# Performance work log

Measured on AMD Instinct MI355X. Metric: run time of the kernel, lower is better.

The kernel has to match this reference:

```python
import jax, jax.numpy as jnp
import numpy as np

# Bone edge list (0-indexed) from _calc_length_single, in original order.
_BONES = np.array([
    (3, 2), (2, 20), (20, 8), (8, 9), (9, 10), (10, 11),
    (20, 4), (4, 5), (5, 6), (6, 7),
    (20, 1), (1, 0), (0, 16), (16, 17), (17, 18), (18, 19),
    (0, 12), (12, 13), (13, 14), (14, 15),
], dtype=np.int32)
_A = jnp.asarray(_BONES[:, 0])
_B = jnp.asarray(_BONES[:, 1])


def _bone_lengths(joints):
    # joints: [B, 21, 3] -> [B, 20]
    diff = joints[:, _A, :] - joints[:, _B, :]
    return jnp.linalg.norm(diff, axis=-1)


def setup_inputs() -> dict:
    key = jax.random.key(0)
    k1, k2 = jax.random.split(key)
    B = 524288
    pred_joints = jax.random.normal(k1, (B, 21, 3), dtype=jnp.float32)
    gt_joints = jax.random.normal(k2, (B, 21, 3), dtype=jnp.float32)
    return {"pred_joints": pred_joints, "gt_joints": gt_joints}


def reference(pred_joints, gt_joints):
    pred_len = _bone_lengths(pred_joints)   # [B, 20]
    gt_len = _bone_lengths(gt_joints)       # [B, 20]
    rel = jnp.abs(pred_len - gt_len) / gt_len
    # mean over 20 bones per sample, then mean over batch == global mean
    return jnp.mean(rel)
```

## Files before the change

### kernel.cpp

```cpp
#include <hip/hip_runtime.h>
#include <hip/hip_bf16.h>


#define TILE_BYTES   16128
#define TILE_PAD_F   4096
#define NBLOCKS      512

static constexpr int JT0[7] = {3,2,2,20,8,9,10};
static constexpr int JT1[7] = {10,11,20,4,5,6,7};
static constexpr int JT2[7] = {20,1,1,0,16,17,18};
static constexpr int JT3[7] = {18,19,0,12,13,14,15};
static constexpr int EA[5] = {0,2,3,4,5};
static constexpr int EB[5] = {1,3,4,5,6};

typedef __attribute__((address_space(1))) const void gvoid_t;
typedef __attribute__((address_space(3))) void lvoid_t;

template<int G>
__device__ __forceinline__ float bone_group(const float* __restrict__ SP,
                                            const float* __restrict__ SG) {
    float px[7], py[7], pz[7], qx[7], qy[7], qz[7];
    #pragma unroll
    for (int k = 0; k < 7; ++k) {
        const int o = 3 * ((G == 0) ? JT0[k] : (G == 1) ? JT1[k] : (G == 2) ? JT2[k] : JT3[k]);
        px[k] = SP[o + 0]; py[k] = SP[o + 1]; pz[k] = SP[o + 2];
        qx[k] = SG[o + 0]; qy[k] = SG[o + 1]; qz[k] = SG[o + 2];
    }
    float s = 0.0f;
    #pragma unroll
    for (int e = 0; e < 5; ++e) {
        const int a = EA[e], b = EB[e];
        float dx = px[a] - px[b];
        float dy = py[a] - py[b];
        float dz = pz[a] - pz[b];
        float pl = sqrtf(dx * dx + dy * dy + dz * dz);
        float ex = qx[a] - qx[b];
        float ey = qy[a] - qy[b];
        float ez = qz[a] - qz[b];
        float gl = sqrtf(ex * ex + ey * ey + ez * ez);
        s += fabsf(pl - gl) / gl;
    }
    return s;
}

__global__ __launch_bounds__(256)
void jll_kernel(const float* __restrict__ pred,
                const float* __restrict__ gt,
                float* __restrict__ partials,
                int tiles_per_block) {
    __shared__ __align__(16) float lds[2][2][TILE_PAD_F];
    __shared__ float wsum[4];

    const int tid  = threadIdx.x;
    const int wave = tid >> 6;
    const int lane = tid & 63;

    const size_t tile0 = (size_t)blockIdx.x * tiles_per_block;

    auto STAGE = [&](int q, size_t tile) {
        const char* srcP = (const char*)pred + tile * (size_t)TILE_BYTES;
        const char* srcG = (const char*)gt   + tile * (size_t)TILE_BYTES;
        #pragma unroll
        for (int c = 0; c < 4; ++c) {
            const int chunk = wave * 4 + c;
            int off = chunk * 1024 + lane * 16;
            if (off > TILE_BYTES - 16) off = TILE_BYTES - 16;
            __builtin_amdgcn_global_load_lds(
                (gvoid_t*)(srcP + off), (lvoid_t*)&lds[q][0][chunk * 256], 16, 0, 0);
            __builtin_amdgcn_global_load_lds(
                (gvoid_t*)(srcG + off), (lvoid_t*)&lds[q][1][chunk * 256], 16, 0, 0);
        }
    };

    float sum = 0.0f;

    STAGE(0, tile0);

    for (int t = 0; t < tiles_per_block; ++t) {
        if (t + 1 < tiles_per_block) {
            STAGE((t + 1) & 1, tile0 + t + 1);
            asm volatile("s_waitcnt vmcnt(8)\n\ts_barrier" ::: "memory");
        } else {
            asm volatile("s_waitcnt vmcnt(0)\n\ts_barrier" ::: "memory");
        }
        __builtin_amdgcn_sched_barrier(0);

        {
            const float* SP = &lds[t & 1][0][lane * 63];
            const float* SG = &lds[t & 1][1][lane * 63];
            float ts;
            if      (wave == 0) ts = bone_group<0>(SP, SG);
            else if (wave == 1) ts = bone_group<1>(SP, SG);
            else if (wave == 2) ts = bone_group<2>(SP, SG);
            else                ts = bone_group<3>(SP, SG);
            sum += ts;
        }

        asm volatile("s_waitcnt lgkmcnt(0)\n\ts_barrier" ::: "memory");
    }

    #pragma unroll
    for (int off = 32; off > 0; off >>= 1)
        sum += __shfl_down(sum, off);

    if (lane == 0) wsum[wave] = sum;
    __syncthreads();
    if (tid == 0)
        partials[blockIdx.x] = wsum[0] + wsum[1] + wsum[2] + wsum[3];
}

__global__ __launch_bounds__(256)
void jll_final_kernel(const float* __restrict__ partials, int nparts,
                      float* __restrict__ out, float inv_count) {
    const int tid = threadIdx.x;
    float sum = 0.0f;
    for (int i = tid; i < nparts; i += 256) sum += partials[i];

    #pragma unroll
    for (int off = 32; off > 0; off >>= 1)
        sum += __shfl_down(sum, off);

    __shared__ float wsum[4];
    const int lane = tid & 63;
    const int wid  = tid >> 6;
    if (lane == 0) wsum[wid] = sum;
    __syncthreads();
    if (tid == 0)
        out[0] = (wsum[0] + wsum[1] + wsum[2] + wsum[3]) * inv_count;
}

extern "C" void kernel_launch(void* const* d_in, const int* in_sizes, int n_in,
                              void* d_out, int out_size, void* d_ws, size_t ws_size,
                              hipStream_t stream) {
    const float* pred = (const float*)d_in[0];
    const float* gt   = (const float*)d_in[1];
    float* out = (float*)d_out;
    float* partials = (float*)d_ws;

    const int nsamples = in_sizes[0] / 63;
    const int ntiles   = nsamples / 64;
    const int tiles_per_block = ntiles / NBLOCKS;

    jll_kernel<<<NBLOCKS, 256, 0, stream>>>(pred, gt, partials, tiles_per_block);

    const float inv_count = 1.0f / ((float)nsamples * 20.0f);
    jll_final_kernel<<<1, 256, 0, stream>>>(partials, NBLOCKS, out, inv_count);
}
```

Before: 47.75 us.

## Halve grid size, peel last pipeline iteration, shrink final reduction to one wave

Reduces the main grid from 512 to 256 blocks, so each block streams twice as many tiles through its double-buffered LDS pipeline. The last tile is peeled out of the loop so the steady-state loop has no branch on the wait count. The final reduction kernel becomes a single 64-thread wave with no LDS or barrier. With 256 blocks on a GPU with 256 CUs, each CU runs only one block, which can lower memory-level parallelism and bandwidth use.

```diff
diff --git a/kernel.cpp b/kernel.cpp
--- a/kernel.cpp
+++ b/kernel.cpp
@@ -4,7 +4,7 @@
 
 #define TILE_BYTES   16128
 #define TILE_PAD_F   4096
-#define NBLOCKS      512
+#define NBLOCKS      256
 
 static constexpr int JT0[7] = {3,2,2,20,8,9,10};
 static constexpr int JT1[7] = {10,11,20,4,5,6,7};
@@ -72,32 +72,32 @@
         }
     };
 
+    auto COMPUTE = [&](int q) -> float {
+        const float* SP = &lds[q][0][lane * 63];
+        const float* SG = &lds[q][1][lane * 63];
+        float ts;
+        if      (wave == 0) ts = bone_group<0>(SP, SG);
+        else if (wave == 1) ts = bone_group<1>(SP, SG);
+        else if (wave == 2) ts = bone_group<2>(SP, SG);
+        else                ts = bone_group<3>(SP, SG);
+        return ts;
+    };
+
     float sum = 0.0f;
 
     STAGE(0, tile0);
 
-    for (int t = 0; t < tiles_per_block; ++t) {
-        if (t + 1 < tiles_per_block) {
-            STAGE((t + 1) & 1, tile0 + t + 1);
-            asm volatile("s_waitcnt vmcnt(8)\n\ts_barrier" ::: "memory");
-        } else {
-            asm volatile("s_waitcnt vmcnt(0)\n\ts_barrier" ::: "memory");
-        }
-        __builtin_amdgcn_sched_barrier(0);
+    for (int t = 0; t < tiles_per_block - 1; ++t) {
+        STAGE((t + 1) & 1, tile0 + t + 1);
+        asm volatile("s_waitcnt vmcnt(8)\n\ts_barrier" ::: "memory");
 
-        {
-            const float* SP = &lds[t & 1][0][lane * 63];
-            const float* SG = &lds[t & 1][1][lane * 63];
-            float ts;
-            if      (wave == 0) ts = bone_group<0>(SP, SG);
-            else if (wave == 1) ts = bone_group<1>(SP, SG);
-            else if (wave == 2) ts = bone_group<2>(SP, SG);
-            else                ts = bone_group<3>(SP, SG);
-            sum += ts;
-        }
+        sum += COMPUTE(t & 1);
 
         asm volatile("s_waitcnt lgkmcnt(0)\n\ts_barrier" ::: "memory");
     }
+
+    asm volatile("s_waitcnt vmcnt(0)\n\ts_barrier" ::: "memory");
+    sum += COMPUTE((tiles_per_block - 1) & 1);
 
     #pragma unroll
     for (int off = 32; off > 0; off >>= 1)
@@ -109,24 +109,19 @@
         partials[blockIdx.x] = wsum[0] + wsum[1] + wsum[2] + wsum[3];
 }
 
-__global__ __launch_bounds__(256)
+__global__ __launch_bounds__(64)
 void jll_final_kernel(const float* __restrict__ partials, int nparts,
                       float* __restrict__ out, float inv_count) {
-    const int tid = threadIdx.x;
+    const int lane = threadIdx.x;
     float sum = 0.0f;
-    for (int i = tid; i < nparts; i += 256) sum += partials[i];
+    for (int i = lane; i < nparts; i += 64) sum += partials[i];
 
     #pragma unroll
     for (int off = 32; off > 0; off >>= 1)
         sum += __shfl_down(sum, off);
 
-    __shared__ float wsum[4];
-    const int lane = tid & 63;
-    const int wid  = tid >> 6;
-    if (lane == 0) wsum[wid] = sum;
-    __syncthreads();
-    if (tid == 0)
-        out[0] = (wsum[0] + wsum[1] + wsum[2] + wsum[3]) * inv_count;
+    if (lane == 0)
+        out[0] = sum * inv_count;
 }
 
 extern "C" void kernel_launch(void* const* d_in, const int* in_sizes, int n_in,
@@ -144,5 +139,5 @@
     jll_kernel<<<NBLOCKS, 256, 0, stream>>>(pred, gt, partials, tiles_per_block);
 
     const float inv_count = 1.0f / ((float)nsamples * 20.0f);
-    jll_final_kernel<<<1, 256, 0, stream>>>(partials, NBLOCKS, out, inv_count);
+    jll_final_kernel<<<1, 64, 0, stream>>>(partials, NBLOCKS, out, inv_count);
 }
```

Measured after the change: 69.25 us. +45.0%, slower.
